# Kernel tuning notes

Hardware: AMD Instinct MI355X
Metric: run time of the kernel (lower is better)

## Reference

```python
import jax, jax.numpy as jnp
import numpy as np

N, E, D, EDIM = 50000, 800000, 128, 1
LN_EPS = 1e-5
NORM_FACTOR = 1.0


def _ln(x, g, b):
    m = jnp.mean(x, axis=-1, keepdims=True)
    v = jnp.var(x, axis=-1, keepdims=True)
    return (x - m) * jax.lax.rsqrt(v + LN_EPS) * g + b


def _mlp(x, w1, b1, g, be, w2, b2):
    # Linear -> SiLU -> LayerNorm -> Linear (matches nn.Sequential in msg_net/out_net)
    h = jax.nn.silu(x @ w1 + b1)
    h = _ln(h, g, be)
    return h @ w2 + b2


def setup_inputs() -> dict:
    key = jax.random.key(0)
    ks = jax.random.split(key, 24)
    s = 1.0 / np.sqrt(D)
    sa = 1.0 / np.sqrt(2 * D + EDIM)
    f32 = jnp.float32
    return {
        "h": jax.random.normal(ks[0], (N, D), f32),
        "edge_attr": jax.random.uniform(ks[1], (E, EDIM), f32),
        "row": jax.random.randint(ks[2], (E,), 0, N),
        "col": jax.random.randint(ks[3], (E,), 0, N),
        "node_mask": jnp.ones((N, 1), f32),
        "edge_mask": jnp.ones((E, 1), f32),
        "lin_w": jax.random.normal(ks[4], (D, D), f32) * s,
        "lin_b": jnp.zeros((D,), f32),
        "msg_w1": jax.random.normal(ks[5], (D, D), f32) * s,
        "msg_b1": jnp.zeros((D,), f32),
        "msg_ln_g": jnp.ones((D,), f32),
        "msg_ln_b": jnp.zeros((D,), f32),
        "msg_w2": jax.random.normal(ks[6], (D, D), f32) * s,
        "msg_b2": jnp.zeros((D,), f32),
        "att_w1": jax.random.normal(ks[7], (2 * D + EDIM, D), f32) * sa,
        "att_b1": jnp.zeros((D,), f32),
        "att_w2": jax.random.normal(ks[8], (D, 1), f32) * s,
        "att_b2": jnp.zeros((1,), f32),
        "out_w1": jax.random.normal(ks[9], (D, D), f32) * s,
        "out_b1": jnp.zeros((D,), f32),
        "out_ln_g": jnp.ones((D,), f32),
        "out_ln_b": jnp.zeros((D,), f32),
        "out_w2": jax.random.normal(ks[10], (D, D), f32) * s,
        "out_b2": jnp.zeros((D,), f32),
        "ln_g": jnp.ones((D,), f32),
        "ln_b": jnp.zeros((D,), f32),
    }


def reference(h, edge_attr, row, col, node_mask, edge_mask,
              lin_w, lin_b,
              msg_w1, msg_b1, msg_ln_g, msg_ln_b, msg_w2, msg_b2,
              att_w1, att_b1, att_w2, att_b2,
              out_w1, out_b1, out_ln_g, out_ln_b, out_w2, out_b2,
              ln_g, ln_b):
    # h = self.linear(h)
    x = h @ lin_w + lin_b                                    # [N, D]
    # msg_net transform of node features
    x_ = _mlp(x, msg_w1, msg_b1, msg_ln_g, msg_ln_b, msg_w2, msg_b2)
    # DenseAtt: cat(x[row], x[col], edge_attr) -> MLP -> sigmoid -> * edge_mask
    feat = jnp.concatenate([x[row], x[col], edge_attr], axis=1)   # [E, 2D+edge_dim]
    att = jax.nn.sigmoid(jax.nn.silu(feat @ att_w1 + att_b1) @ att_w2 + att_b2)
    att = att * edge_mask                                    # [E, 1]
    # gather -> weighted message -> scatter_add (unsorted_segment_sum, 'sum' norm)
    msg = jax.ops.segment_sum(x_[col] * att, row, num_segments=N) / NORM_FACTOR
    # out_net transform, residual, final LayerNorm
    msg = _mlp(msg, out_w1, out_b1, out_ln_g, out_ln_b, out_w2, out_b2)
    return _ln(x + msg, ln_g, ln_b)                          # [N, D]
```

## Files before the change

kernel.cpp:

```cpp
#include <hip/hip_runtime.h>

#define LN_EPS 1e-5f

typedef __attribute__((ext_vector_type(8))) short short8;
typedef __attribute__((ext_vector_type(4))) float f32x4;

__device__ __forceinline__ float sigf(float x) {
    return __builtin_amdgcn_rcpf(1.0f + __expf(-x));
}

__device__ __forceinline__ unsigned short f2bf(float f) {
    unsigned u = __float_as_uint(f);
    return (unsigned short)((u + 0x7fffu + ((u >> 16) & 1u)) >> 16);
}
__device__ __forceinline__ unsigned f2bf2(float lo, float hi) {
    return (unsigned)f2bf(lo) | ((unsigned)f2bf(hi) << 16);
}
__device__ __forceinline__ void bf2f(unsigned u, float& lo, float& hi) {
    lo = __uint_as_float(u << 16);
    hi = __uint_as_float(u & 0xffff0000u);
}
__device__ __forceinline__ void bf8f(uint4 p, float* o) {
    bf2f(p.x, o[0], o[1]); bf2f(p.y, o[2], o[3]);
    bf2f(p.z, o[4], o[5]); bf2f(p.w, o[6], o[7]);
}
__device__ __forceinline__ float bf1f(unsigned short s) {
    return __uint_as_float(((unsigned)s) << 16);
}

__device__ __forceinline__ float quad_add_all(float x) {
    int v = __builtin_amdgcn_update_dpp(0, __float_as_int(x), 0xB1, 0xF, 0xF, true);
    x += __int_as_float(v);
    v = __builtin_amdgcn_update_dpp(0, __float_as_int(x), 0x4E, 0xF, 0xF, true);
    x += __int_as_float(v);
    return x;
}

__global__ __launch_bounds__(256)
void prep_w(const float* __restrict__ lin_w, const float* __restrict__ msg_w1,
            const float* __restrict__ msg_w2, const float* __restrict__ att_w1,
            const float* __restrict__ out_w1, const float* __restrict__ out_w2,
            const float* __restrict__ att_b1, const float* __restrict__ att_w2,
            unsigned short* __restrict__ wp, float* __restrict__ bias256,
            unsigned* __restrict__ wpk)
{
    const int idx = blockIdx.x * 256 + threadIdx.x;
    if (idx < 8 * 16384) {
        const int m = idx >> 14, r = idx & 16383;
        const int k = r >> 7, n = r & 127;
        const float* src; int slot; int fnBase = 0;
        switch (m) {
            case 0: src = lin_w;  slot = 0; break;
            case 1: src = msg_w1; slot = 1; break;
            case 2: src = msg_w2; slot = 2; break;
            case 3: src = att_w1; slot = 3; break;
            case 4: src = att_w1 + 128 * 128; slot = 3; fnBase = 8; break;
            case 5: src = out_w1; slot = 5; break;
            default: src = out_w2; slot = 6; break;
        }
        const float v = src[k * 128 + n];
        const int fn = fnBase + (n >> 4);
        const int fk = k >> 5, kb = (k >> 3) & 3, j = k & 7;
        const size_t dst = (size_t)slot * 16384 + ((size_t)((fn * 4 + fk) * 64 + (n & 15) + 16 * kb)) * 8 + j;
        wp[dst] = f2bf(v);
    } else if (idx < 8 * 16384 + 256) {
        const int t = idx - 8 * 16384;
        bias256[t] = (t < 128) ? att_b1[t] : 0.f;
    } else if (idx < 8 * 16384 + 256 + 128) {
        const int t = idx - (8 * 16384 + 256);
        wpk[t] = (unsigned)f2bf(att_w1[256 * 128 + t]) | ((unsigned)f2bf(att_w2[t]) << 16);
    }
}

__device__ __forceinline__ short8 ldA_f32(const float* A, size_t row, int k0) {
    const float* ap = A + row * 128 + k0;
    const float4 f0 = *(const float4*)ap;
    const float4 f1 = *(const float4*)(ap + 4);
    union { unsigned u[4]; short8 s; } v;
    v.u[0] = f2bf2(f0.x, f0.y); v.u[1] = f2bf2(f0.z, f0.w);
    v.u[2] = f2bf2(f1.x, f1.y); v.u[3] = f2bf2(f1.z, f1.w);
    return v.s;
}
__device__ __forceinline__ short8 ldA_bf(const unsigned short* A, size_t row, int k0) {
    return *(const short8*)(A + row * 128 + k0);
}

__global__ __launch_bounds__(256, 3)
void front_mfma(const float* __restrict__ h,
                const unsigned short* __restrict__ wp, const float* __restrict__ lin_b,
                const float* __restrict__ att_b1,
                const float* __restrict__ msg_b1,
                const float* __restrict__ m1g, const float* __restrict__ m1b,
                const float* __restrict__ msg_b2,
                unsigned short* __restrict__ xbH, unsigned short* __restrict__ xrH,
                unsigned short* __restrict__ xcH, unsigned short* __restrict__ xmH,
                int nrows)
{
    __shared__ uint4 Bbuf[2048];
    __shared__ unsigned short hof[4 * 2048];
    const int tid = threadIdx.x;
    const int w = tid >> 6, lane = tid & 63;
    const int r0 = blockIdx.x * 64;
    const int arow = r0 + w * 16 + (lane & 15);
    const size_t rowc = (arow < nrows) ? (size_t)arow : (size_t)(nrows - 1);
    const int kh = (lane >> 4) * 8;
    const int cn = lane & 15, rq = lane >> 4;
    unsigned short* hw = hof + w * 2048;
    const short8* Bf = (const short8*)Bbuf;

    short8 a[4];
#pragma unroll
    for (int fk = 0; fk < 4; ++fk) a[fk] = ldA_f32(h, rowc, fk * 32 + kh);

    const uint4* wp4 = (const uint4*)wp;

#define LOADB(slotoff)  { _Pragma("unroll") \
    for (int i = 0; i < 8; ++i) Bbuf[tid + i * 256] = wp4[(slotoff) + tid + i * 256]; }

#define MFMA8(afrag, accv) { _Pragma("unroll") \
    for (int fk = 0; fk < 4; ++fk) { _Pragma("unroll") \
        for (int fn = 0; fn < 8; ++fn) \
            accv[fn] = __builtin_amdgcn_mfma_f32_16x16x32_bf16(afrag[fk], Bf[(fn * 4 + fk) * 64 + lane], accv[fn], 0, 0, 0); } }

#define EPI_HOF(accv, bvv) { _Pragma("unroll") \
    for (int reg = 0; reg < 4; ++reg) { \
        const int row16 = rq * 4 + reg; const int sw = (row16 & 7) << 3; _Pragma("unroll") \
        for (int fn = 0; fn < 8; ++fn) \
            hw[row16 * 128 + ((fn * 16 + cn) ^ sw)] = f2bf(accv[fn][reg] + bvv[fn]); } }

#define FLUSH(G) { const int frow = lane >> 2; const int fgr = r0 + w * 16 + frow; \
    const int fsw = (frow & 7) << 3; _Pragma("unroll") \
    for (int it = 0; it < 4; ++it) { \
        const int c0 = ((lane & 3) + it * 4) * 8; \
        short8 v = *(const short8*)(hw + frow * 128 + (c0 ^ fsw)); \
        if (fgr < nrows) *(short8*)((G) + (size_t)fgr * 128 + c0) = v; } }

    LOADB(0);
    __syncthreads();
    f32x4 acc[8];
#pragma unroll
    for (int fn = 0; fn < 8; ++fn) acc[fn] = (f32x4){0.f, 0.f, 0.f, 0.f};
    MFMA8(a, acc);
    {
        float bv[8];
#pragma unroll
        for (int fn = 0; fn < 8; ++fn) bv[fn] = lin_b[fn * 16 + cn];
        EPI_HOF(acc, bv);
    }
    short8 ax[4];
    {
        const int row16 = lane & 15;
        const int sw = (row16 & 7) << 3;
#pragma unroll
        for (int fk = 0; fk < 4; ++fk)
            ax[fk] = *(const short8*)(hw + row16 * 128 + ((fk * 32 + kh) ^ sw));
    }
    FLUSH(xbH);
    __syncthreads();

    LOADB(3 * 2048);
    __syncthreads();
#pragma unroll
    for (int fn = 0; fn < 8; ++fn) acc[fn] = (f32x4){0.f, 0.f, 0.f, 0.f};
    MFMA8(ax, acc);
    {
        float bv[8];
#pragma unroll
        for (int fn = 0; fn < 8; ++fn) bv[fn] = att_b1[fn * 16 + cn];
        EPI_HOF(acc, bv);
    }
    FLUSH(xrH);
    __syncthreads();

    LOADB(4 * 2048);
    __syncthreads();
#pragma unroll
    for (int fn = 0; fn < 8; ++fn) acc[fn] = (f32x4){0.f, 0.f, 0.f, 0.f};
    MFMA8(ax, acc);
    {
        float bv[8];
#pragma unroll
        for (int fn = 0; fn < 8; ++fn) bv[fn] = 0.f;
        EPI_HOF(acc, bv);
    }
    FLUSH(xcH);
    __syncthreads();

    LOADB(1 * 2048);
    __syncthreads();
#pragma unroll
    for (int fn = 0; fn < 8; ++fn) acc[fn] = (f32x4){0.f, 0.f, 0.f, 0.f};
    MFMA8(ax, acc);
    {
        float bv[8], gv[8], bbv[8];
#pragma unroll
        for (int fn = 0; fn < 8; ++fn) {
            bv[fn] = msg_b1[fn * 16 + cn]; gv[fn] = m1g[fn * 16 + cn]; bbv[fn] = m1b[fn * 16 + cn];
        }
#pragma unroll
        for (int reg = 0; reg < 4; ++reg) {
            float val[8];
            float sum = 0.f, sq = 0.f;
#pragma unroll
            for (int fn = 0; fn < 8; ++fn) {
                float v = acc[fn][reg] + bv[fn];
                v = v * sigf(v);
                val[fn] = v; sum += v; sq += v * v;
            }
#pragma unroll
            for (int m = 1; m < 16; m <<= 1) { sum += __shfl_xor(sum, m); sq += __shfl_xor(sq, m); }
            const float mean = sum * (1.f / 128.f);
            const float var = sq * (1.f / 128.f) - mean * mean;
            const float rstd = rsqrtf(var + LN_EPS);
            const int row16 = rq * 4 + reg;
            const int sw = (row16 & 7) << 3;
#pragma unroll
            for (int fn = 0; fn < 8; ++fn) {
                const float o = (val[fn] - mean) * rstd * gv[fn] + bbv[fn];
                hw[row16 * 128 + ((fn * 16 + cn) ^ sw)] = f2bf(o);
            }
        }
    }
    short8 am[4];
    {
        const int row16 = lane & 15;
        const int sw = (row16 & 7) << 3;
#pragma unroll
        for (int fk = 0; fk < 4; ++fk)
            am[fk] = *(const short8*)(hw + row16 * 128 + ((fk * 32 + kh) ^ sw));
    }
    __syncthreads();

    LOADB(2 * 2048);
    __syncthreads();
#pragma unroll
    for (int fn = 0; fn < 8; ++fn) acc[fn] = (f32x4){0.f, 0.f, 0.f, 0.f};
    MFMA8(am, acc);
    {
        float bv[8];
#pragma unroll
        for (int fn = 0; fn < 8; ++fn) bv[fn] = msg_b2[fn * 16 + cn];
        EPI_HOF(acc, bv);
    }
    FLUSH(xmH);
#undef LOADB
#undef MFMA8
#undef EPI_HOF
#undef FLUSH
}

__global__ __launch_bounds__(256, 4)
void gemm2_mfma(const unsigned short* __restrict__ Av,
                const unsigned short* __restrict__ Wp1, const float* __restrict__ b1,
                const float* __restrict__ ln1g, const float* __restrict__ ln1b,
                const unsigned short* __restrict__ Wp2, const float* __restrict__ b2,
                const float* __restrict__ ln2g, const float* __restrict__ ln2b,
                const unsigned short* __restrict__ resH, float* __restrict__ Cf, int nrows)
{
    __shared__ unsigned short hof[4 * 2048];
    const int tid = threadIdx.x;
    const int w = tid >> 6, lane = tid & 63;
    const int r0 = blockIdx.x * 64;
    const int arow = r0 + w * 16 + (lane & 15);
    const size_t rowc = (arow < nrows) ? (size_t)arow : (size_t)(nrows - 1);
    const int kh = (lane >> 4) * 8;
    const int cn = lane & 15, rq = lane >> 4;

    short8 a[4];
#pragma unroll
    for (int fk = 0; fk < 4; ++fk) a[fk] = ldA_bf(Av, rowc, fk * 32 + kh);

    const short8* B1f = (const short8*)Wp1;
    f32x4 acc[8];
#pragma unroll
    for (int fn = 0; fn < 8; ++fn) acc[fn] = (f32x4){0.f, 0.f, 0.f, 0.f};
#pragma unroll
    for (int fk = 0; fk < 4; ++fk)
#pragma unroll
        for (int fn = 0; fn < 8; ++fn)
            acc[fn] = __builtin_amdgcn_mfma_f32_16x16x32_bf16(a[fk], B1f[(fn * 4 + fk) * 64 + lane], acc[fn], 0, 0, 0);

    unsigned short* hw = hof + w * 2048;
    {
        float bv[8], gv[8], bbv[8];
#pragma unroll
        for (int fn = 0; fn < 8; ++fn) {
            bv[fn] = b1[fn * 16 + cn]; gv[fn] = ln1g[fn * 16 + cn]; bbv[fn] = ln1b[fn * 16 + cn];
        }
#pragma unroll
        for (int reg = 0; reg < 4; ++reg) {
            float val[8];
            float sum = 0.f, sq = 0.f;
#pragma unroll
            for (int fn = 0; fn < 8; ++fn) {
                float v = acc[fn][reg] + bv[fn];
                v = v * sigf(v);
                val[fn] = v; sum += v; sq += v * v;
            }
#pragma unroll
            for (int m = 1; m < 16; m <<= 1) { sum += __shfl_xor(sum, m); sq += __shfl_xor(sq, m); }
            const float mean = sum * (1.f / 128.f);
            const float var = sq * (1.f / 128.f) - mean * mean;
            const float rstd = rsqrtf(var + LN_EPS);
            const int row16 = rq * 4 + reg;
            const int sw = (row16 & 7) << 3;
#pragma unroll
            for (int fn = 0; fn < 8; ++fn) {
                const float o = (val[fn] - mean) * rstd * gv[fn] + bbv[fn];
                hw[row16 * 128 + ((fn * 16 + cn) ^ sw)] = f2bf(o);
            }
        }
    }

    short8 a2[4];
    {
        const int row16 = lane & 15;
        const int sw = (row16 & 7) << 3;
#pragma unroll
        for (int fk = 0; fk < 4; ++fk)
            a2[fk] = *(const short8*)(hw + row16 * 128 + ((fk * 32 + kh) ^ sw));
    }

    const short8* B2f = (const short8*)Wp2;
    f32x4 acc2[8];
#pragma unroll
    for (int fn = 0; fn < 8; ++fn) acc2[fn] = (f32x4){0.f, 0.f, 0.f, 0.f};
#pragma unroll
    for (int fk = 0; fk < 4; ++fk)
#pragma unroll
        for (int fn = 0; fn < 8; ++fn)
            acc2[fn] = __builtin_amdgcn_mfma_f32_16x16x32_bf16(a2[fk], B2f[(fn * 4 + fk) * 64 + lane], acc2[fn], 0, 0, 0);

    float bv2[8], gv[8], bbv[8];
#pragma unroll
    for (int fn = 0; fn < 8; ++fn) {
        bv2[fn] = b2[fn * 16 + cn]; gv[fn] = ln2g[fn * 16 + cn]; bbv[fn] = ln2b[fn * 16 + cn];
    }
#pragma unroll
    for (int reg = 0; reg < 4; ++reg) {
        const int gr = r0 + w * 16 + rq * 4 + reg;
        const int grc = gr < nrows ? gr : nrows - 1;
        float val[8];
        float sum = 0.f, sq = 0.f;
#pragma unroll
        for (int fn = 0; fn < 8; ++fn) {
            float v = acc2[fn][reg] + bv2[fn] + bf1f(resH[(size_t)grc * 128 + fn * 16 + cn]);
            val[fn] = v; sum += v; sq += v * v;
        }
#pragma unroll
        for (int m = 1; m < 16; m <<= 1) { sum += __shfl_xor(sum, m); sq += __shfl_xor(sq, m); }
        const float mean = sum * (1.f / 128.f);
        const float var = sq * (1.f / 128.f) - mean * mean;
        const float rstd = rsqrtf(var + LN_EPS);
        if (gr < nrows) {
#pragma unroll
            for (int fn = 0; fn < 8; ++fn)
                Cf[(size_t)gr * 128 + fn * 16 + cn] = (val[fn] - mean) * rstd * gv[fn] + bbv[fn];
        }
    }
}

__global__ __launch_bounds__(256)
void hist_rank(const int* __restrict__ row, int* __restrict__ cnt,
               int* __restrict__ rank, int E)
{
    const int tid = blockIdx.x * blockDim.x + threadIdx.x;
    const int stride = gridDim.x * blockDim.x;
    for (int e0 = tid; e0 < E; e0 += stride * 8) {
        int r[8]; bool val[8];
#pragma unroll
        for (int u = 0; u < 8; ++u) {
            const int e = e0 + u * stride;
            val[u] = e < E;
            r[u] = val[u] ? row[e] : 0;
        }
        int rk[8];
#pragma unroll
        for (int u = 0; u < 8; ++u)
            if (val[u]) rk[u] = atomicAdd(&cnt[r[u]], 1);
#pragma unroll
        for (int u = 0; u < 8; ++u)
            if (val[u]) rank[e0 + u * stride] = rk[u];
    }
}

__global__ __launch_bounds__(1024)
void scan_a(const int* __restrict__ cnt, int* __restrict__ off,
            int* __restrict__ btot, int n)
{
    __shared__ int wsum[16];
    const int tid = threadIdx.x, lane = tid & 63, wv = tid >> 6;
    const int i = blockIdx.x * 1024 + tid;
    const int v = (i < n) ? cnt[i] : 0;
    int incl = v;
#pragma unroll
    for (int d = 1; d < 64; d <<= 1) { int t = __shfl_up(incl, d); if (lane >= d) incl += t; }
    if (lane == 63) wsum[wv] = incl;
    __syncthreads();
    if (tid == 0) {
        int run = 0;
        for (int ww = 0; ww < 16; ++ww) { int t = wsum[ww]; wsum[ww] = run; run += t; }
    }
    __syncthreads();
    if (i < n) off[i] = wsum[wv] + incl - v;
    if (tid == 1023) btot[blockIdx.x] = wsum[15] + incl;
}

__global__ __launch_bounds__(64)
void scan_b(int* __restrict__ btot, int* __restrict__ bexc,
            int* __restrict__ off, int n, int nb, int E)
{
    const int t = threadIdx.x;
    const int v = (t < nb) ? btot[t] : 0;
    int incl = v;
#pragma unroll
    for (int d = 1; d < 64; d <<= 1) { int u = __shfl_up(incl, d); if (t >= d) incl += u; }
    if (t < nb) bexc[t] = incl - v;
    if (t == 0) off[n] = E;
}

__global__ __launch_bounds__(1024)
void scan_c(int* __restrict__ off, const int* __restrict__ bexc, int n)
{
    const int i = blockIdx.x * 1024 + threadIdx.x;
    if (i < n) off[i] += bexc[blockIdx.x];
}

__global__ __launch_bounds__(256, 4)
void att_edge(const unsigned short* __restrict__ xrH,
              const unsigned short* __restrict__ xcH,
              const int* __restrict__ row, const int* __restrict__ col,
              const float* __restrict__ ea, const float* __restrict__ em,
              const int* __restrict__ rank, const int* __restrict__ off,
              const unsigned* __restrict__ wpk, const float* __restrict__ b2p,
              uint2* __restrict__ catS, int E)
{
    const int lane = threadIdx.x & 63;
    const int q = lane & 3;
    const int gwid = (blockIdx.x * blockDim.x + threadIdx.x) >> 6;
    const int nw = (gridDim.x * blockDim.x) >> 6;

    unsigned wk[32];
#pragma unroll
    for (int ch = 0; ch < 4; ++ch) {
        const uint4 k0 = ((const uint4*)wpk)[ch * 8 + q * 2];
        const uint4 k1 = ((const uint4*)wpk)[ch * 8 + q * 2 + 1];
        wk[ch * 8 + 0] = k0.x; wk[ch * 8 + 1] = k0.y; wk[ch * 8 + 2] = k0.z; wk[ch * 8 + 3] = k0.w;
        wk[ch * 8 + 4] = k1.x; wk[ch * 8 + 5] = k1.y; wk[ch * 8 + 6] = k1.z; wk[ch * 8 + 7] = k1.w;
    }
    const float b2 = *b2p;

    for (int base = gwid * 16; base < E; base += nw * 16) {
        const int e = base + (lane >> 2);
        const bool valid = e < E;
        const int ec = valid ? e : E - 1;
        const int r = row[ec], c = col[ec];
        const float eax = ea[ec], emv = em[ec];
        const unsigned short* xr = xrH + (size_t)r * 128 + q * 8;
        const unsigned short* xc = xcH + (size_t)c * 128 + q * 8;

        uint4 pa[4], pb[4];
#pragma unroll
        for (int ch = 0; ch < 4; ++ch) {
            pa[ch] = *(const uint4*)(xr + ch * 32);
            pb[ch] = *(const uint4*)(xc + ch * 32);
        }

        float pc[4];
#pragma unroll
        for (int ch = 0; ch < 4; ++ch) {
            float xa[8], xb[8];
            bf8f(pa[ch], xa); bf8f(pb[ch], xb);
            float s = 0.f;
#pragma unroll
            for (int i = 0; i < 8; ++i) {
                const unsigned wv = wk[ch * 8 + i];
                const float weF = __uint_as_float(wv << 16);
                const float w2F = __uint_as_float(wv & 0xffff0000u);
                const float t = xa[i] + xb[i] + eax * weF;
                s += t * sigf(t) * w2F;
            }
            pc[ch] = s;
        }
        float p = (pc[0] + pc[1]) + (pc[2] + pc[3]);
        p = quad_add_all(p);
        const float att = sigf(p + b2) * emv;
        if (valid && q == 0) {
            const int pos = off[r] + rank[ec];
            catS[pos] = make_uint2((unsigned)c, __float_as_uint(att));
        }
    }
}

__global__ __launch_bounds__(256)
void accum_k(const unsigned short* __restrict__ xmH, const int* __restrict__ off,
             const uint2* __restrict__ catS, unsigned short* __restrict__ msgH, int N)
{
    const int lane = threadIdx.x & 63;
    const int g = lane >> 4, l = lane & 15;
    const int gwid = (blockIdx.x * blockDim.x + threadIdx.x) >> 6;
    const int nw = (gridDim.x * blockDim.x) >> 6;
    const uint4* xm4 = (const uint4*)xmH;

    for (int wid = gwid; wid < N; wid += nw) {
        int j0 = off[wid];
        const int jend = off[wid + 1];
        float acc[8] = {0.f, 0.f, 0.f, 0.f, 0.f, 0.f, 0.f, 0.f};

        for (; j0 + 16 <= jend; j0 += 16) {
            uint2 ca[4]; uint4 pk[4];
#pragma unroll
            for (int u = 0; u < 4; ++u) ca[u] = catS[j0 + u * 4 + g];
#pragma unroll
            for (int u = 0; u < 4; ++u) pk[u] = xm4[(size_t)ca[u].x * 16 + l];
#pragma unroll
            for (int u = 0; u < 4; ++u) {
                const float att = __uint_as_float(ca[u].y);
                float xm[8];
                bf8f(pk[u], xm);
#pragma unroll
                for (int i = 0; i < 8; ++i) acc[i] = fmaf(att, xm[i], acc[i]);
            }
        }
        for (; j0 + 8 <= jend; j0 += 8) {
            const uint2 caA = catS[j0 + g];
            const uint2 caB = catS[j0 + 4 + g];
            const uint4 pA = xm4[(size_t)caA.x * 16 + l];
            const uint4 pB = xm4[(size_t)caB.x * 16 + l];
            const float attA = __uint_as_float(caA.y);
            const float attB = __uint_as_float(caB.y);
            float xmA[8], xmB[8];
            bf8f(pA, xmA); bf8f(pB, xmB);
#pragma unroll
            for (int i = 0; i < 8; ++i)
                acc[i] = fmaf(attB, xmB[i], fmaf(attA, xmA[i], acc[i]));
        }
        for (; j0 < jend; j0 += 4) {
            const int je = j0 + g;
            const bool valid = je < jend;
            const int jc = valid ? je : jend - 1;
            const uint2 ca = catS[jc];
            const uint4 p = xm4[(size_t)ca.x * 16 + l];
            const float att = valid ? __uint_as_float(ca.y) : 0.f;
            float xm[8];
            bf8f(p, xm);
#pragma unroll
            for (int i = 0; i < 8; ++i) acc[i] = fmaf(att, xm[i], acc[i]);
        }

#pragma unroll
        for (int i = 0; i < 8; ++i) {
            acc[i] += __shfl_xor(acc[i], 16);
            acc[i] += __shfl_xor(acc[i], 32);
        }
        if (g == 0) {
            uint4 pk;
            pk.x = f2bf2(acc[0], acc[1]); pk.y = f2bf2(acc[2], acc[3]);
            pk.z = f2bf2(acc[4], acc[5]); pk.w = f2bf2(acc[6], acc[7]);
            ((uint4*)msgH)[(size_t)wid * 16 + l] = pk;
        }
    }
}

extern "C" void kernel_launch(void* const* d_in, const int* in_sizes, int n_in,
                              void* d_out, int out_size, void* d_ws, size_t ws_size,
                              hipStream_t stream)
{
    const float* h        = (const float*)d_in[0];
    const float* edge_attr= (const float*)d_in[1];
    const int*   row      = (const int*)d_in[2];
    const int*   col      = (const int*)d_in[3];
    const float* edge_mask= (const float*)d_in[5];
    const float* lin_w    = (const float*)d_in[6];
    const float* lin_b    = (const float*)d_in[7];
    const float* msg_w1   = (const float*)d_in[8];
    const float* msg_b1   = (const float*)d_in[9];
    const float* msg_ln_g = (const float*)d_in[10];
    const float* msg_ln_b = (const float*)d_in[11];
    const float* msg_w2   = (const float*)d_in[12];
    const float* msg_b2   = (const float*)d_in[13];
    const float* att_w1   = (const float*)d_in[14];
    const float* att_b1   = (const float*)d_in[15];
    const float* att_w2   = (const float*)d_in[16];
    const float* att_b2   = (const float*)d_in[17];
    const float* out_w1   = (const float*)d_in[18];
    const float* out_b1   = (const float*)d_in[19];
    const float* out_ln_g = (const float*)d_in[20];
    const float* out_ln_b = (const float*)d_in[21];
    const float* out_w2   = (const float*)d_in[22];
    const float* out_b2   = (const float*)d_in[23];
    const float* ln_g     = (const float*)d_in[24];
    const float* ln_b     = (const float*)d_in[25];

    const int N = in_sizes[0] / 128;
    const int E = in_sizes[2];
    const size_t NF = (size_t)N * 128;

    unsigned short* xbH  = (unsigned short*)d_ws;
    unsigned short* xrH  = xbH + NF;
    unsigned short* xcH  = xrH + NF;
    unsigned short* xmH  = xcH + NF;
    unsigned short* msgH = xmH + NF;
    int*    cnt   = (int*)(msgH + NF);
    int*    off   = cnt + N;
    int*    btot  = off + N + 8;
    int*    bexc  = btot + 64;
    int*    rank  = bexc + 64;
    uint2*  catS  = (uint2*)(rank + E);
    unsigned short* wp = (unsigned short*)(catS + E);
    float* bias256 = (float*)(wp + 8 * 16384);
    unsigned* wpk  = (unsigned*)(bias256 + 256);

    const int gb = (N + 63) / 64;
    const int nb = (N + 1023) / 1024;
    const int hgrid = (E + 256 * 8 - 1) / (256 * 8);

    prep_w<<<514, 256, 0, stream>>>(lin_w, msg_w1, msg_w2, att_w1, out_w1, out_w2,
                                    att_b1, att_w2, wp, bias256, wpk);
    hipMemsetAsync(cnt, 0, (size_t)N * sizeof(int), stream);
    hist_rank<<<hgrid, 256, 0, stream>>>(row, cnt, rank, E);
    scan_a<<<nb, 1024, 0, stream>>>(cnt, off, btot, N);
    scan_b<<<1, 64, 0, stream>>>(btot, bexc, off, N, nb, E);
    scan_c<<<nb, 1024, 0, stream>>>(off, bexc, N);

    front_mfma<<<gb, 256, 0, stream>>>(h, wp, lin_b, att_b1,
                                       msg_b1, msg_ln_g, msg_ln_b, msg_b2,
                                       xbH, xrH, xcH, xmH, N);

    att_edge<<<2048, 256, 0, stream>>>(xrH, xcH, row, col, edge_attr, edge_mask,
                                       rank, off, wpk, att_b2, catS, E);

    accum_k<<<2048, 256, 0, stream>>>(xmH, off, catS, msgH, N);

    gemm2_mfma<<<gb, 256, 0, stream>>>(msgH, wp + 5 * 16384, out_b1, out_ln_g, out_ln_b,
                                       wp + 6 * 16384, out_b2, ln_g, ln_b,
                                       xbH, (float*)d_out, N);
}
```

Before: 204.3 us.

## Prefetch weight tiles into registers and software-pipeline edge index loads

In the fused node GEMM kernel, each next weight slice is now loaded from global memory into registers while the current MFMA stage runs, then written to LDS after the barrier. This hides the global-load latency that previously sat between barriers. In the edge attention kernel, the row, col, edge-attribute, mask, rank and offset loads for the next edge batch are issued before the current batch's compute, which removes dependent load latency from the critical path. Both changes raise register pressure, which could lower occupancy.

```diff
diff --git a/kernel.cpp b/kernel.cpp
--- a/kernel.cpp
+++ b/kernel.cpp
@@ -107,15 +107,15 @@
     const int cn = lane & 15, rq = lane >> 4;
     unsigned short* hw = hof + w * 2048;
     const short8* Bf = (const short8*)Bbuf;
-
-    short8 a[4];
-#pragma unroll
-    for (int fk = 0; fk < 4; ++fk) a[fk] = ldA_f32(h, rowc, fk * 32 + kh);
-
     const uint4* wp4 = (const uint4*)wp;
 
-#define LOADB(slotoff)  { _Pragma("unroll") \
-    for (int i = 0; i < 8; ++i) Bbuf[tid + i * 256] = wp4[(slotoff) + tid + i * 256]; }
+    uint4 wreg[8];
+
+#define PREF(slotoff) { _Pragma("unroll") \
+    for (int i = 0; i < 8; ++i) wreg[i] = wp4[(slotoff) + tid + i * 256]; }
+
+#define WRITEB() { _Pragma("unroll") \
+    for (int i = 0; i < 8; ++i) Bbuf[tid + i * 256] = wreg[i]; }
 
 #define MFMA8(afrag, accv) { _Pragma("unroll") \
     for (int fk = 0; fk < 4; ++fk) { _Pragma("unroll") \
@@ -135,9 +135,16 @@
         short8 v = *(const short8*)(hw + frow * 128 + (c0 ^ fsw)); \
         if (fgr < nrows) *(short8*)((G) + (size_t)fgr * 128 + c0) = v; } }
 
-    LOADB(0);
-    __syncthreads();
+    short8 a[4];
+#pragma unroll
+    for (int fk = 0; fk < 4; ++fk) a[fk] = ldA_f32(h, rowc, fk * 32 + kh);
+
     f32x4 acc[8];
+
+    PREF(0);
+    WRITEB();
+    __syncthreads();
+    PREF(3 * 2048);
 #pragma unroll
     for (int fn = 0; fn < 8; ++fn) acc[fn] = (f32x4){0.f, 0.f, 0.f, 0.f};
     MFMA8(a, acc);
@@ -158,8 +165,9 @@
     FLUSH(xbH);
     __syncthreads();
 
-    LOADB(3 * 2048);
-    __syncthreads();
+    WRITEB();
+    __syncthreads();
+    PREF(4 * 2048);
 #pragma unroll
     for (int fn = 0; fn < 8; ++fn) acc[fn] = (f32x4){0.f, 0.f, 0.f, 0.f};
     MFMA8(ax, acc);
@@ -172,8 +180,9 @@
     FLUSH(xrH);
     __syncthreads();
 
-    LOADB(4 * 2048);
-    __syncthreads();
+    WRITEB();
+    __syncthreads();
+    PREF(1 * 2048);
 #pragma unroll
     for (int fn = 0; fn < 8; ++fn) acc[fn] = (f32x4){0.f, 0.f, 0.f, 0.f};
     MFMA8(ax, acc);
@@ -186,8 +195,9 @@
     FLUSH(xcH);
     __syncthreads();
 
-    LOADB(1 * 2048);
-    __syncthreads();
+    WRITEB();
+    __syncthreads();
+    PREF(2 * 2048);
 #pragma unroll
     for (int fn = 0; fn < 8; ++fn) acc[fn] = (f32x4){0.f, 0.f, 0.f, 0.f};
     MFMA8(ax, acc);
@@ -231,7 +241,7 @@
     }
     __syncthreads();
 
-    LOADB(2 * 2048);
+    WRITEB();
     __syncthreads();
 #pragma unroll
     for (int fn = 0; fn < 8; ++fn) acc[fn] = (f32x4){0.f, 0.f, 0.f, 0.f};
@@ -243,7 +253,8 @@
         EPI_HOF(acc, bv);
     }
     FLUSH(xmH);
-#undef LOADB
+#undef PREF
+#undef WRITEB
 #undef MFMA8
 #undef EPI_HOF
 #undef FLUSH
@@ -450,20 +461,38 @@
     }
     const float b2 = *b2p;
 
-    for (int base = gwid * 16; base < E; base += nw * 16) {
-        const int e = base + (lane >> 2);
-        const bool valid = e < E;
-        const int ec = valid ? e : E - 1;
-        const int r = row[ec], c = col[ec];
-        const float eax = ea[ec], emv = em[ec];
+    int base = gwid * 16;
+    if (base >= E) return;
+
+    int e = base + (lane >> 2);
+    bool valid = e < E;
+    int ec = valid ? e : E - 1;
+    int r = row[ec], c = col[ec];
+    float eax = ea[ec], emv = em[ec];
+    int rk = rank[ec], ofr = off[r];
+
+    while (true) {
         const unsigned short* xr = xrH + (size_t)r * 128 + q * 8;
         const unsigned short* xc = xcH + (size_t)c * 128 + q * 8;
-
         uint4 pa[4], pb[4];
 #pragma unroll
         for (int ch = 0; ch < 4; ++ch) {
             pa[ch] = *(const uint4*)(xr + ch * 32);
             pb[ch] = *(const uint4*)(xc + ch * 32);
+        }
+
+        const int nbase = base + nw * 16;
+        const bool more = nbase < E;
+        int r2 = 0, c2 = 0, rk2 = 0, ofr2 = 0;
+        float eax2 = 0.f, emv2 = 0.f;
+        bool valid2 = false;
+        if (more) {
+            const int e2 = nbase + (lane >> 2);
+            valid2 = e2 < E;
+            const int ec2 = valid2 ? e2 : E - 1;
+            r2 = row[ec2]; c2 = col[ec2];
+            eax2 = ea[ec2]; emv2 = em[ec2];
+            rk2 = rank[ec2]; ofr2 = off[r2];
         }
 
         float pc[4];
@@ -485,10 +514,12 @@
         float p = (pc[0] + pc[1]) + (pc[2] + pc[3]);
         p = quad_add_all(p);
         const float att = sigf(p + b2) * emv;
-        if (valid && q == 0) {
-            const int pos = off[r] + rank[ec];
-            catS[pos] = make_uint2((unsigned)c, __float_as_uint(att));
-        }
+        if (valid && q == 0)
+            catS[ofr + rk] = make_uint2((unsigned)c, __float_as_uint(att));
+
+        if (!more) break;
+        base = nbase;
+        valid = valid2; r = r2; c = c2; eax = eax2; emv = emv2; rk = rk2; ofr = ofr2;
     }
 }
 
```

Result: slower. 232.3 us (+13.7%).
